# Optimization experiments

Measured on AMD Instinct MI355X. Metric: run time of the kernel, lower is better.

Reference implementation:

```python
import jax, jax.numpy as jnp
import numpy as np

B=1; NW=8; SEG=511; S=NW*(SEG+1); W=256; C=S//W; H=12; D=64; DM=768; FF=3072; V=50265; L=12; OUT=128; G=NW
SCALE = float(1.0/np.sqrt(D))
GPOS = np.arange(NW)*(S//NW)                      # global (CLS) token positions
IDX = np.arange(C)[:,None]*W + np.arange(3*W)[None,:]   # [C,3W] gather into padded key seq
_band = np.abs(np.arange(3*W)[None,:]-np.arange(W)[:,None]-W) <= W   # [W,3W] |rel|<=W band
_kpos = IDX - W
LMASK = _band[None] & ((_kpos>=0)&(_kpos<S))[:,None,:]  # [C,W,3W]

def _ln(x, s, b):
    m = jnp.mean(x, -1, keepdims=True)
    v = jnp.mean((x-m)**2, -1, keepdims=True)
    return (x-m)*jax.lax.rsqrt(v+1e-5)*s + b

def _layer(h, Wq,bq,Wk,bk,Wv,bv,Wo,bo,Wqg,bqg,Wkg,bkg,Wvg,bvg,l1s,l1b,W1,b1,W2,b2,l2s,l2b):
    hd = lambda z: z.reshape(B,S,H,D).transpose(0,2,1,3)   # [B,H,S,D]
    q = hd(h@Wq+bq)*SCALE
    k = hd(h@Wk+bk); v = hd(h@Wv+bv)
    kc = jnp.pad(k, ((0,0),(0,0),(W,W),(0,0)))[:,:,IDX]    # [B,H,C,3W,D]
    vc = jnp.pad(v, ((0,0),(0,0),(W,W),(0,0)))[:,:,IDX]
    qc = q.reshape(B,H,C,W,D)
    # banded local scores + scores to global keys, joint softmax (HF longformer style)
    sl = jnp.where(LMASK, jnp.einsum('bhcqd,bhckd->bhcqk', qc, kc), -1e9)
    sg = jnp.einsum('bhcqd,bhgd->bhcqg', qc, k[:,:,GPOS])
    a = jax.nn.softmax(jnp.concatenate([sg, sl], -1), -1)  # [B,H,C,W,G+3W]
    out = jnp.einsum('bhcqg,bhgd->bhcqd', a[..., :G], v[:,:,GPOS]) \
        + jnp.einsum('bhcqk,bhckd->bhcqd', a[..., G:], vc)
    out = out.reshape(B,H,S,D)
    # global tokens: full attention with separate global projections, overwrite their outputs
    qg = (h[:,GPOS]@Wqg+bqg).reshape(B,G,H,D).transpose(0,2,1,3)*SCALE
    ag = jax.nn.softmax(jnp.einsum('bhgd,bhsd->bhgs', qg, hd(h@Wkg+bkg)), -1)
    out = out.at[:,:,GPOS,:].set(jnp.einsum('bhgs,bhsd->bhgd', ag, hd(h@Wvg+bvg)))
    y = out.transpose(0,2,1,3).reshape(B,S,DM)@Wo + bo
    h = _ln(h + y, l1s, l1b)
    return _ln(h + jax.nn.gelu(h@W1+b1)@W2 + b2, l2s, l2b)

def setup_inputs() -> dict:
    keys = iter(jax.random.split(jax.random.key(0), 64))
    p = lambda *s: jax.random.normal(next(keys), s, jnp.float32)*0.02
    d = {"x": jax.random.randint(next(keys), (B, NW*SEG), 0, V),
         "word_emb": p(V, DM), "pos_emb": p(S, DM),
         "emb_ln_s": jnp.ones((DM,)), "emb_ln_b": jnp.zeros((DM,))}
    for n in ["Wq","Wk","Wv","Wo","Wqg","Wkg","Wvg"]:
        d[n] = p(L, DM, DM); d["b"+n[1:]] = jnp.zeros((L, DM))
    d["ln1_s"]=jnp.ones((L,DM)); d["ln1_b"]=jnp.zeros((L,DM))
    d["W1"]=p(L,DM,FF); d["b1"]=jnp.zeros((L,FF))
    d["W2"]=p(L,FF,DM); d["b2"]=jnp.zeros((L,DM))
    d["ln2_s"]=jnp.ones((L,DM)); d["ln2_b"]=jnp.zeros((L,DM))
    d["Wout"]=p(DM,OUT); d["bout"]=jnp.zeros((OUT,))
    return d

def reference(x, word_emb, pos_emb, emb_ln_s, emb_ln_b, Wq, bq, Wk, bk, Wv, bv, Wo, bo,
              Wqg, bqg, Wkg, bkg, Wvg, bvg, ln1_s, ln1_b, W1, b1, W2, b2, ln2_s, ln2_b,
              Wout, bout):
    # prepend CLS (id 0) per window -> S=4096 token ids
    ids = jnp.concatenate([jnp.zeros((B, NW, 1), x.dtype), x.reshape(B, NW, SEG)], 2).reshape(B, S)
    h = _ln(word_emb[ids] + pos_emb[None], emb_ln_s, emb_ln_b)
    for l in range(L):
        h = _layer(h, Wq[l],bq[l],Wk[l],bk[l],Wv[l],bv[l],Wo[l],bo[l],
                   Wqg[l],bqg[l],Wkg[l],bkg[l],Wvg[l],bvg[l],
                   ln1_s[l],ln1_b[l],W1[l],b1[l],W2[l],b2[l],ln2_s[l],ln2_b[l])
    return h[:, GPOS] @ Wout + bout   # cls_pooling + output head: [B, NW, OUT]
```

## Files before the change

### kernel.cpp

```cpp
#include <hip/hip_runtime.h>
#include <hip/hip_bf16.h>


typedef unsigned short u16;
typedef __attribute__((ext_vector_type(4))) float floatx4;
typedef __attribute__((ext_vector_type(4))) unsigned int uintx4;
typedef __attribute__((ext_vector_type(8))) short bf16x8;
typedef __attribute__((ext_vector_type(4))) u16 u16x4;

#define S_LEN 4096
#define QKVG_N 4608
#define NL 12

__device__ inline u16 f2bf(float x) {
    union { __hip_bfloat16 b; u16 u; } cv;
    cv.b = __float2bfloat16(x);
    return cv.u;
}
__device__ inline float bf2f(u16 u) {
    union { float f; unsigned int i; } c; c.i = ((unsigned int)u) << 16; return c.f;
}
__device__ inline float gelu_f(float x) {
    float x3 = x * x * x;
    return 0.5f * x * (1.0f + tanhf(0.7978845608028654f * (x + 0.044715f * x3)));
}

#define GLDS16(g, l)                                                              \
    __builtin_amdgcn_global_load_lds(                                             \
        (const __attribute__((address_space(1))) unsigned int*)(g),               \
        (__attribute__((address_space(3))) unsigned int*)(l), 16, 0, 0)

__global__ __launch_bounds__(256) void prep_weights_k(
    const float* __restrict__ Wq0, const float* __restrict__ Wk0, const float* __restrict__ Wv0,
    const float* __restrict__ Wkg0, const float* __restrict__ Wvg0, const float* __restrict__ Wqg0,
    const float* __restrict__ Wo0, const float* __restrict__ W10, const float* __restrict__ W20,
    const float* __restrict__ bq0, const float* __restrict__ bk0, const float* __restrict__ bv0,
    const float* __restrict__ bkg0, const float* __restrict__ bvg0, const float* __restrict__ bqg0,
    u16* __restrict__ wTall, float* __restrict__ bcatall)
{
    const int t = threadIdx.x;
    const int bid = blockIdx.x;
    if (bid >= 6480) {
        int i = (bid - 6480) * 256 + t;
        int l = i / 4608, j = i - l * 4608;
        float v;
        if (j < 768)       v = bq0[l * 768 + j];
        else if (j < 1536) v = bk0[l * 768 + j - 768];
        else if (j < 2304) v = bv0[l * 768 + j - 1536];
        else if (j < 3072) v = bkg0[l * 768 + j - 2304];
        else if (j < 3840) v = bvg0[l * 768 + j - 3072];
        else               v = bqg0[l * 768 + j - 3840];
        bcatall[(size_t)l * 4608 + j] = v;
        return;
    }

    const int l = bid / 540, b = bid - l * 540;
    const size_t sqo = (size_t)l * 589824;
    const size_t sff = (size_t)l * 2359296;
    u16* wq = wTall + (size_t)l * 8847360;
    const float* src; u16* dst; int K, N, kt, ns;
    if (b < 216) {
        int m = b / 36, s = b - m * 36;
        src = ((m == 0) ? Wq0 : (m == 1) ? Wk0 : (m == 2) ? Wv0 :
               (m == 3) ? Wkg0 : (m == 4) ? Wvg0 : Wqg0) + sqo;
        dst = wq + (size_t)m * 589824;
        K = 768; N = 768; kt = s / 3; ns = s - kt * 3;
    } else if (b < 252) {
        int s = b - 216; src = Wo0 + sqo; dst = wq + 3538944;
        K = 768; N = 768; kt = s / 3; ns = s - kt * 3;
    } else if (b < 396) {
        int s = b - 252; src = W10 + sff; dst = wq + 4128768;
        K = 768; N = 3072; kt = s / 12; ns = s - kt * 12;
    } else {
        int s = b - 396; src = W20 + sff; dst = wq + 6488064;
        K = 3072; N = 768; kt = s / 3; ns = s - kt * 3;
    }
    const int k0 = kt * 64, n0b = ns * 256;

    __shared__ float tb[2][64][65];
    const int r = t >> 4, c4 = (t & 15) * 4;
    const float* srow = src + (size_t)k0 * N + n0b;
    floatx4 rg[4];
    #pragma unroll
    for (int j = 0; j < 4; j++)
        rg[j] = *(const floatx4*)&srow[(size_t)(r + 16 * j) * N + c4];

    #pragma unroll
    for (int s4 = 0; s4 < 4; ++s4) {
        float (*tbb)[65] = tb[s4 & 1];
        #pragma unroll
        for (int j = 0; j < 4; j++) {
            int kk = r + 16 * j;
            #pragma unroll
            for (int i = 0; i < 4; i++) tbb[c4 + i][kk] = rg[j][i];
        }
        __syncthreads();
        if (s4 < 3) {
            #pragma unroll
            for (int j = 0; j < 4; j++)
                rg[j] = *(const floatx4*)&srow[(size_t)(r + 16 * j) * N + (s4 + 1) * 64 + c4];
        }
        int n0 = n0b + s4 * 64;
        #pragma unroll
        for (int j = 0; j < 4; j++) {
            int n = r + 16 * j;
            u16x4 o;
            #pragma unroll
            for (int i = 0; i < 4; i++) o[i] = f2bf(tbb[n][c4 + i]);
            *(u16x4*)&dst[(size_t)(n0 + n) * K + k0 + c4] = o;
        }
    }
}

template <int ACT, int WF, int WB, int SKIPQG, int WVT, int SPLITB>
__global__ __launch_bounds__(256, 3) void gemm_k(
    const u16* __restrict__ A, const u16* __restrict__ Bt,
    const float* __restrict__ bias,
    float* __restrict__ Cf, u16* __restrict__ Cb, u16* __restrict__ vTg,
    int N, int K, int lda, int ldb)
{
    int lin = blockIdx.y * 32 + blockIdx.x;
    int qq = gridDim.y << 2;
    int wg = (lin & 7) * qq + (lin >> 3);
    int bx = wg & 31, by = wg >> 5;
    if (SKIPQG && by >= 30 && (bx & 3) != 0) return;
    int bm = bx * 128, bn = by * 128;
    const int zoff = SPLITB ? blockIdx.z : 0;
    const u16* Ab = A + (size_t)zoff * K;
    const u16* Bb = Bt + (size_t)zoff * K;
    float* Cfz = WF ? Cf + (size_t)zoff * S_LEN * N : (float*)nullptr;

    __shared__ __align__(16) u16 As[128][64];
    __shared__ __align__(16) u16 Bs[128][64];
    int t = threadIdx.x, lane = t & 63, wv = t >> 6;
    int wm = (wv >> 1) * 64, wn = (wv & 1) * 64;
    int srow = t >> 3, scol = (t & 7) * 8;
    int fr = lane & 15, fo = (lane >> 4) * 8;

    floatx4 acc[4][4];
    #pragma unroll
    for (int i = 0; i < 4; i++)
        #pragma unroll
        for (int j = 0; j < 4; j++) acc[i][j] = (floatx4){0.f, 0.f, 0.f, 0.f};

    const int nk = K >> 6;
    for (int kt = 0; kt < nk; ++kt) {
        const u16* ag = Ab + (size_t)(bm + srow) * lda + kt * 64 + scol;
        const u16* bg = Bb + (size_t)(bn + srow) * ldb + kt * 64 + scol;
        #pragma unroll
        for (int c = 0; c < 4; ++c) {
            GLDS16(ag + (size_t)(32 * c) * lda, &As[srow + 32 * c][scol]);
            GLDS16(bg + (size_t)(32 * c) * ldb, &Bs[srow + 32 * c][scol]);
        }
        __syncthreads();
        #pragma unroll
        for (int ks = 0; ks < 2; ++ks) {
            bf16x8 af[4], bfr[4];
            #pragma unroll
            for (int i = 0; i < 4; i++) af[i]  = *(const bf16x8*)&As[wm + i * 16 + fr][ks * 32 + fo];
            #pragma unroll
            for (int i = 0; i < 4; i++) bfr[i] = *(const bf16x8*)&Bs[wn + i * 16 + fr][ks * 32 + fo];
            #pragma unroll
            for (int i = 0; i < 4; i++)
                #pragma unroll
                for (int j = 0; j < 4; j++)
                    acc[i][j] = __builtin_amdgcn_mfma_f32_16x16x32_bf16(af[i], bfr[j], acc[i][j], 0, 0, 0);
        }
        __syncthreads();
    }

    int dr = (lane >> 4) * 4, dc = lane & 15;
    #pragma unroll
    for (int i = 0; i < 4; i++) {
        #pragma unroll
        for (int j = 0; j < 4; j++) {
            int r0 = bm + wm + i * 16 + dr;
            int cc = bn + wn + j * 16 + dc;
            float bsv = (!SPLITB || blockIdx.z == 0) ? bias[cc] : 0.f;
            u16x4 tv;
            #pragma unroll
            for (int r = 0; r < 4; r++) {
                float v = acc[i][j][r] + bsv;
                if (ACT == 1) v = gelu_f(v);
                if (WF) Cfz[(size_t)(r0 + r) * N + cc] = v;
                if (WB) { u16 b = f2bf(v); Cb[(size_t)(r0 + r) * N + cc] = b; tv[r] = b; }
            }
            if (WVT && cc >= 1536 && cc < 2304)
                *(u16x4*)&vTg[(size_t)(cc - 1536) * 4096 + r0] = tv;
        }
    }
}

__global__ __launch_bounds__(256) void attn_local_k(
    const u16* __restrict__ qkvg, const u16* __restrict__ vTg, u16* __restrict__ aob)
{
    int lin = blockIdx.y * 64 + blockIdx.x;
    int wg = (lin & 7) * 96 + (lin >> 3);
    const int qb = wg & 63, hh = wg >> 6;
    const int t = threadIdx.x, lane = t & 63, w = t >> 6;
    const int g = lane >> 4, qi = lane & 15;
    __shared__ __align__(16) u16 ks[64][72];
    __shared__ __align__(16) u16 vt[64][72];
    __shared__ __align__(16) u16 pbuf[4][16][40];

    const int q0w = qb * 64 + w * 16;
    const int sq = q0w + qi;

    bf16x8 qf0, qf1;
    {
        const u16* qp = qkvg + (size_t)(q0w + qi) * QKVG_N + hh * 64 + g * 8;
        qf0 = *(const bf16x8*)qp;
        qf1 = *(const bf16x8*)(qp + 32);
    }

    floatx4 acc[4];
    #pragma unroll
    for (int i = 0; i < 4; i++) acc[i] = (floatx4){0.f, 0.f, 0.f, 0.f};
    float mrun = -1e30f, lrun = 0.f;

    for (int tile = 0; tile <= 9; ++tile) {
        const int kbase = qb * 64 - 256 + (tile - 1) * 64;
        if (tile > 0 && (kbase < 0 || kbase >= S_LEN)) continue;
        __syncthreads();
        if (tile == 0) {
            for (int i = t; i < 576; i += 256) ((uintx4*)vt)[i] = (uintx4){0, 0, 0, 0};
            __syncthreads();
            if (t < 64) {
                int gg = t >> 3, d0 = (t & 7) * 8;
                *(uintx4*)&ks[gg][d0] =
                    *(const uintx4*)(qkvg + (size_t)(gg * 512) * QKVG_N + 768 + hh * 64 + d0);
            }
            for (int e = t; e < 512; e += 256) {
                int d = e >> 3, gg = e & 7;
                vt[d][gg] = vTg[(size_t)(hh * 64 + d) * 4096 + gg * 512];
            }
        } else {
            for (int c = t; c < 512; c += 256) {
                int r = c >> 3, c0 = (c & 7) * 8;
                *(uintx4*)&ks[r][c0] =
                    *(const uintx4*)(qkvg + (size_t)(kbase + r) * QKVG_N + 768 + hh * 64 + c0);
                *(uintx4*)&vt[r][c0] =
                    *(const uintx4*)(vTg + (size_t)(hh * 64 + r) * 4096 + kbase + c0);
            }
        }
        __syncthreads();

        const bool gt = (tile == 0);
        const bool edge = (tile == 1) | (tile == 9);
        const int ng = gt ? 1 : 2;
        for (int kg2 = 0; kg2 < ng; ++kg2) {
            floatx4 sf[2];
            sf[1] = (floatx4){0.f, 0.f, 0.f, 0.f};
            {
                bf16x8 ka0 = *(const bf16x8*)&ks[kg2 * 32 + qi][g * 8];
                bf16x8 ka1 = *(const bf16x8*)&ks[kg2 * 32 + qi][32 + g * 8];
                floatx4 z = (floatx4){0.f, 0.f, 0.f, 0.f};
                z = __builtin_amdgcn_mfma_f32_16x16x32_bf16(ka0, qf0, z, 0, 0, 0);
                sf[0] = __builtin_amdgcn_mfma_f32_16x16x32_bf16(ka1, qf1, z, 0, 0, 0);
            }
            if (!gt) {
                bf16x8 kb0 = *(const bf16x8*)&ks[kg2 * 32 + 16 + qi][g * 8];
                bf16x8 kb1 = *(const bf16x8*)&ks[kg2 * 32 + 16 + qi][32 + g * 8];
                floatx4 z = (floatx4){0.f, 0.f, 0.f, 0.f};
                z = __builtin_amdgcn_mfma_f32_16x16x32_bf16(kb0, qf0, z, 0, 0, 0);
                sf[1] = __builtin_amdgcn_mfma_f32_16x16x32_bf16(kb1, qf1, z, 0, 0, 0);
            }
            float p8[8];
            float mloc = -1e30f;
            #pragma unroll
            for (int f = 0; f < 2; ++f)
                #pragma unroll
                for (int r = 0; r < 4; ++r) {
                    int kl = kg2 * 32 + f * 16 + g * 4 + r;
                    float sc = sf[f][r] * 0.125f;
                    if (gt) {
                        if (kl >= 8) sc = -1e30f;
                    } else if (edge) {
                        int dd = kbase + kl - sq;
                        if (dd > 256 || dd < -256) sc = -1e30f;
                    }
                    p8[f * 4 + r] = sc;
                    mloc = fmaxf(mloc, sc);
                }
            mloc = fmaxf(mloc, __shfl_xor(mloc, 16));
            mloc = fmaxf(mloc, __shfl_xor(mloc, 32));
            float mnew = fmaxf(mrun, mloc);
            float alpha = __expf(mrun - mnew);
            mrun = mnew;
            float ls = 0.f;
            #pragma unroll
            for (int i = 0; i < 8; ++i) { float p = __expf(p8[i] - mnew); p8[i] = p; ls += p; }
            ls += __shfl_xor(ls, 16);
            ls += __shfl_xor(ls, 32);
            lrun = lrun * alpha + ls;
            u16x4 w0, w1;
            #pragma unroll
            for (int r = 0; r < 4; ++r) { w0[r] = f2bf(p8[r]); w1[r] = f2bf(p8[4 + r]); }
            *(u16x4*)&pbuf[w][qi][g * 4] = w0;
            *(u16x4*)&pbuf[w][qi][16 + g * 4] = w1;
            float al[4];
            #pragma unroll
            for (int r = 0; r < 4; ++r) al[r] = __shfl(alpha, g * 4 + r);
            #pragma unroll
            for (int dt = 0; dt < 4; ++dt)
                #pragma unroll
                for (int r = 0; r < 4; ++r) acc[dt][r] *= al[r];
            bf16x8 pf = *(const bf16x8*)&pbuf[w][qi][g * 8];
            #pragma unroll
            for (int dt = 0; dt < 4; ++dt) {
                bf16x8 vb = *(const bf16x8*)&vt[dt * 16 + qi][kg2 * 32 + g * 8];
                acc[dt] = __builtin_amdgcn_mfma_f32_16x16x32_bf16(pf, vb, acc[dt], 0, 0, 0);
            }
        }
    }

    float inv = 1.f / lrun;
    float li[4];
    #pragma unroll
    for (int r = 0; r < 4; ++r) li[r] = __shfl(inv, g * 4 + r);
    #pragma unroll
    for (int dt = 0; dt < 4; ++dt)
        #pragma unroll
        for (int r = 0; r < 4; ++r) {
            int s = q0w + g * 4 + r;
            aob[(size_t)s * 768 + hh * 64 + dt * 16 + qi] = f2bf(acc[dt][r] * li[r]);
        }
}

#define BLOCK_MEANVAR(sum, sq, mean, inv)                                        \
    {                                                                            \
        for (int o_ = 32; o_ > 0; o_ >>= 1) {                                    \
            sum += __shfl_down(sum, o_); sq += __shfl_down(sq, o_);              \
        }                                                                        \
        __shared__ float rs_[4], rq_[4];                                         \
        if ((threadIdx.x & 63) == 0) { rs_[threadIdx.x >> 6] = sum; rq_[threadIdx.x >> 6] = sq; } \
        __syncthreads();                                                         \
        float S_ = rs_[0] + rs_[1] + rs_[2] + rs_[3];                            \
        float Q_ = rq_[0] + rq_[1] + rq_[2] + rq_[3];                            \
        mean = S_ * (1.f / 768.f);                                               \
        float var_ = Q_ * (1.f / 768.f) - mean * mean;                           \
        inv = rsqrtf(var_ + 1e-5f);                                              \
    }

__global__ __launch_bounds__(256) void embed_ln_k(
    const int* __restrict__ x, const float* __restrict__ wemb, const float* __restrict__ pemb,
    const float* __restrict__ gs, const float* __restrict__ gb,
    float* __restrict__ hf, u16* __restrict__ hb)
{
    int s = blockIdx.x, t = threadIdx.x;
    int w = s >> 9, p = s & 511;
    int id = (p == 0) ? 0 : x[w * 511 + p - 1];
    float v[3], sum = 0.f, sq = 0.f;
    #pragma unroll
    for (int r = 0; r < 3; r++) {
        int d = t + r * 256;
        float e = wemb[(size_t)id * 768 + d] + pemb[(size_t)s * 768 + d];
        v[r] = e; sum += e; sq += e * e;
    }
    float mean, inv;
    BLOCK_MEANVAR(sum, sq, mean, inv)
    #pragma unroll
    for (int r = 0; r < 3; r++) {
        int d = t + r * 256;
        float y = (v[r] - mean) * inv * gs[d] + gb[d];
        hf[(size_t)s * 768 + d] = y;
        hb[(size_t)s * 768 + d] = f2bf(y);
    }
}

__global__ __launch_bounds__(192) void ln_resid_k(
    const float* __restrict__ xa, const float* __restrict__ yf,
    const float* __restrict__ gs, const float* __restrict__ gb,
    float* __restrict__ of, u16* __restrict__ ob)
{
    int s = blockIdx.x, t = threadIdx.x;
    size_t off = (size_t)s * 768 + t * 4;
    floatx4 v = *(const floatx4*)(xa + off);
    #pragma unroll
    for (int z = 0; z < 4; z++) {
        floatx4 b = *(const floatx4*)(yf + (size_t)z * 4096 * 768 + off);
        #pragma unroll
        for (int i = 0; i < 4; i++) v[i] += b[i];
    }
    float sum = v[0] + v[1] + v[2] + v[3];
    float sq = v[0] * v[0] + v[1] * v[1] + v[2] * v[2] + v[3] * v[3];
    #pragma unroll
    for (int o = 32; o > 0; o >>= 1) {
        sum += __shfl_down(sum, o); sq += __shfl_down(sq, o);
    }
    __shared__ float rs_[3], rq_[3];
    if ((t & 63) == 0) { rs_[t >> 6] = sum; rq_[t >> 6] = sq; }
    __syncthreads();
    float S = rs_[0] + rs_[1] + rs_[2];
    float Q = rq_[0] + rq_[1] + rq_[2];
    float mean = S * (1.f / 768.f);
    float inv = rsqrtf(Q * (1.f / 768.f) - mean * mean + 1e-5f);
    floatx4 g4 = *(const floatx4*)(gs + t * 4);
    floatx4 b4 = *(const floatx4*)(gb + t * 4);
    floatx4 y;
    u16x4 o4;
    #pragma unroll
    for (int i = 0; i < 4; i++) {
        y[i] = (v[i] - mean) * inv * g4[i] + b4[i];
        o4[i] = f2bf(y[i]);
    }
    *(floatx4*)(of + off) = y;
    *(u16x4*)(ob + off) = o4;
}

__global__ __launch_bounds__(256) void attn_gpart_k(
    const u16* __restrict__ qkvg,
    float* __restrict__ pacc, float* __restrict__ pm, float* __restrict__ pl)
{
    const int hh = blockIdx.x, ck = blockIdx.y;
    const int t = threadIdx.x;
    __shared__ float qs[8][64];
    __shared__ __align__(16) u16 ks[128][72];
    __shared__ __align__(16) u16 vs[128][64];
    __shared__ float sc[8][128];
    __shared__ float mred[8], lred[8];

    for (int i = t; i < 512; i += 256) {
        int g = i >> 6, d = i & 63;
        qs[g][d] = bf2f(qkvg[(size_t)(g * 512) * QKVG_N + 3840 + hh * 64 + d]) * 0.125f;
    }
    const int s0 = ck * 128;
    for (int u = t; u < 1024; u += 256) {
        int r = u >> 3, c = u & 7;
        const u16* src = qkvg + (size_t)(s0 + r) * QKVG_N + hh * 64 + c * 8;
        *(uintx4*)&ks[r][c * 8] = *(const uintx4*)(src + 2304);
        *(uintx4*)&vs[r][c * 8] = *(const uintx4*)(src + 3072);
    }
    __syncthreads();

    {
        int key = t & 127, q0 = (t >> 7) * 4;
        float a[4] = {0.f, 0.f, 0.f, 0.f};
        #pragma unroll
        for (int c = 0; c < 8; ++c) {
            uintx4 pk = *(const uintx4*)&ks[key][c * 8];
            const u16* uu = (const u16*)&pk;
            #pragma unroll
            for (int e = 0; e < 8; ++e) {
                float kv = bf2f(uu[e]);
                #pragma unroll
                for (int q = 0; q < 4; ++q) a[q] += kv * qs[q0 + q][c * 8 + e];
            }
        }
        #pragma unroll
        for (int q = 0; q < 4; ++q) sc[q0 + q][key] = a[q];
    }
    __syncthreads();

    {
        int q = t >> 5, lq = t & 31;
        float m = -1e30f;
        #pragma unroll
        for (int i = 0; i < 4; ++i) m = fmaxf(m, sc[q][lq + i * 32]);
        #pragma unroll
        for (int o = 1; o < 32; o <<= 1) m = fmaxf(m, __shfl_xor(m, o));
        float ls = 0.f;
        #pragma unroll
        for (int i = 0; i < 4; ++i) {
            float p = __expf(sc[q][lq + i * 32] - m);
            sc[q][lq + i * 32] = p; ls += p;
        }
        #pragma unroll
        for (int o = 1; o < 32; o <<= 1) ls += __shfl_xor(ls, o);
        if (lq == 0) { mred[q] = m; lred[q] = ls; }
    }
    __syncthreads();

    {
        int d = t & 63, qb = t >> 6;
        float a0 = 0.f, a1 = 0.f;
        #pragma unroll 4
        for (int s = 0; s < 128; ++s) {
            float v = bf2f(vs[s][d]);
            a0 += sc[qb][s] * v;
            a1 += sc[qb + 4][s] * v;
        }
        float* pb = pacc + (((size_t)hh * 32 + ck) * 8) * 64;
        pb[qb * 64 + d] = a0;
        pb[(qb + 4) * 64 + d] = a1;
        if (t < 8) {
            pm[((size_t)hh * 32 + ck) * 8 + t] = mred[t];
            pl[((size_t)hh * 32 + ck) * 8 + t] = lred[t];
        }
    }
}

__global__ __launch_bounds__(64) void attn_gred_k(
    const float* __restrict__ pacc, const float* __restrict__ pm,
    const float* __restrict__ pl, u16* __restrict__ aob)
{
    int hh = blockIdx.x, gq = blockIdx.y;
    int d = threadIdx.x;
    float M = -1e30f;
    #pragma unroll 4
    for (int c = 0; c < 32; ++c)
        M = fmaxf(M, pm[((size_t)hh * 32 + c) * 8 + gq]);
    float L = 0.f, o = 0.f;
    #pragma unroll 4
    for (int c = 0; c < 32; ++c) {
        float w = __expf(pm[((size_t)hh * 32 + c) * 8 + gq] - M);
        L += pl[((size_t)hh * 32 + c) * 8 + gq] * w;
        o += w * pacc[(((size_t)hh * 32 + c) * 8 + gq) * 64 + d];
    }
    aob[(size_t)(gq * 512) * 768 + hh * 64 + d] = f2bf(o / L);
}

__global__ __launch_bounds__(128) void head_k(
    const float* __restrict__ hf, const float* __restrict__ Wout,
    const float* __restrict__ bout, float* __restrict__ out)
{
    int g = blockIdx.x, n = threadIdx.x;
    __shared__ float hsh[768];
    for (int i = n; i < 768; i += 128) hsh[i] = hf[(size_t)(g * 512) * 768 + i];
    __syncthreads();
    float a = 0.f;
    #pragma unroll 4
    for (int k = 0; k < 768; k++) a += hsh[k] * Wout[k * 128 + n];
    out[g * 128 + n] = a + bout[n];
}

extern "C" void kernel_launch(void* const* d_in, const int* in_sizes, int n_in,
                              void* d_out, int out_size, void* d_ws, size_t ws_size,
                              hipStream_t stream)
{
    (void)in_sizes; (void)n_in; (void)out_size; (void)ws_size;
    const int*   x    = (const int*)  d_in[0];
    const float* wemb = (const float*)d_in[1];
    const float* pemb = (const float*)d_in[2];
    const float* elns = (const float*)d_in[3];
    const float* elnb = (const float*)d_in[4];
    const float* Wq   = (const float*)d_in[5];
    const float* bq   = (const float*)d_in[6];
    const float* Wk   = (const float*)d_in[7];
    const float* bk   = (const float*)d_in[8];
    const float* Wv   = (const float*)d_in[9];
    const float* bv   = (const float*)d_in[10];
    const float* Wo   = (const float*)d_in[11];
    const float* bo   = (const float*)d_in[12];
    const float* Wqg  = (const float*)d_in[13];
    const float* bqg  = (const float*)d_in[14];
    const float* Wkg  = (const float*)d_in[15];
    const float* bkg  = (const float*)d_in[16];
    const float* Wvg  = (const float*)d_in[17];
    const float* bvg  = (const float*)d_in[18];
    const float* l1s  = (const float*)d_in[19];
    const float* l1b  = (const float*)d_in[20];
    const float* W1   = (const float*)d_in[21];
    const float* b1   = (const float*)d_in[22];
    const float* W2   = (const float*)d_in[23];
    const float* b2   = (const float*)d_in[24];
    const float* l2s  = (const float*)d_in[25];
    const float* l2b  = (const float*)d_in[26];
    const float* Wout = (const float*)d_in[27];
    const float* boutp= (const float*)d_in[28];

    char* W = (char*)d_ws;
    float* hf    = (float*)(W);
    u16*   hb    = (u16*)  (W + 12582912);
    u16*   qkvg  = (u16*)  (W + 18874368);
    u16*   ff1b  = (u16*)  (W + 18874368);
    u16*   vTg   = (u16*)  (W + 56623104);
    u16*   aob   = (u16*)  (W + 62914560);
    float* yf    = (float*)(W + 69206016);
    float* pacc  = (float*)(W + 119537664);
    float* pmw   = (float*)(W + 120324096);
    float* plw   = (float*)(W + 120336384);
    float* bcatall = (float*)(W + 120348672);
    u16*   wTall = (u16*)  (W + 120569856);

    prep_weights_k<<<6696, 256, 0, stream>>>(
        Wq, Wk, Wv, Wkg, Wvg, Wqg, Wo, W1, W2,
        bq, bk, bv, bkg, bvg, bqg, wTall, bcatall);

    embed_ln_k<<<4096, 256, 0, stream>>>(x, wemb, pemb, elns, elnb, hf, hb);

    for (int l = 0; l < NL; ++l) {
        u16* wTl      = wTall + (size_t)l * 8847360;
        u16* wqkvgT_l = wTl;
        u16* woT_l    = wTl + 3538944;
        u16* w1T_l    = woT_l + 589824;
        u16* w2T_l    = w1T_l + 2359296;
        float* bcat_l = bcatall + (size_t)l * 4608;
        const float* bo_l  = bo  + (size_t)l * 768;
        const float* b1_l  = b1  + (size_t)l * 3072;
        const float* b2_l  = b2  + (size_t)l * 768;
        const float* l1s_l = l1s + (size_t)l * 768;
        const float* l1b_l = l1b + (size_t)l * 768;
        const float* l2s_l = l2s + (size_t)l * 768;
        const float* l2b_l = l2b + (size_t)l * 768;

        gemm_k<0, 0, 1, 1, 1, 0><<<dim3(32, 36), 256, 0, stream>>>(
            hb, wqkvgT_l, bcat_l, (float*)nullptr, qkvg, vTg, QKVG_N, 768, 768, 768);

        attn_local_k<<<dim3(64, 12), 256, 0, stream>>>(qkvg, vTg, aob);

        attn_gpart_k<<<dim3(12, 32), 256, 0, stream>>>(qkvg, pacc, pmw, plw);
        attn_gred_k<<<dim3(12, 8), 64, 0, stream>>>(pacc, pmw, plw, aob);

        gemm_k<0, 1, 0, 0, 0, 1><<<dim3(32, 6, 4), 256, 0, stream>>>(
            aob, woT_l, bo_l, yf, (u16*)nullptr, (u16*)nullptr, 768, 192, 768, 768);
        ln_resid_k<<<4096, 192, 0, stream>>>(hf, yf, l1s_l, l1b_l, hf, hb);

        gemm_k<1, 0, 1, 0, 0, 0><<<dim3(32, 24), 256, 0, stream>>>(
            hb, w1T_l, b1_l, (float*)nullptr, ff1b, (u16*)nullptr, 3072, 768, 768, 768);
        gemm_k<0, 1, 0, 0, 0, 1><<<dim3(32, 6, 4), 256, 0, stream>>>(
            ff1b, w2T_l, b2_l, yf, (u16*)nullptr, (u16*)nullptr, 768, 768, 3072, 3072);
        ln_resid_k<<<4096, 192, 0, stream>>>(hf, yf, l2s_l, l2b_l, hf, hb);
    }

    head_k<<<8, 128, 0, stream>>>(hf, Wout, boutp, (float*)d_out);
}
```

Before: 2.838 ms.

## Reduce split-K GEMM partials with atomics into one zeroed buffer

Split-K GEMM blocks now atomically add their partial results into a single fp32 output buffer instead of writing separate per-split slices. The residual layernorm reads that one buffer and zeroes it afterwards for reuse, and the embedding kernel zeroes it on first use. This cuts the partial-sum write and read traffic, since four separate slices are no longer summed. In exchange it adds atomic contention and makes the summation order, and so the result, nondeterministic.

```diff
diff --git a/kernel.cpp b/kernel.cpp
--- a/kernel.cpp
+++ b/kernel.cpp
@@ -128,7 +128,6 @@
     const int zoff = SPLITB ? blockIdx.z : 0;
     const u16* Ab = A + (size_t)zoff * K;
     const u16* Bb = Bt + (size_t)zoff * K;
-    float* Cfz = WF ? Cf + (size_t)zoff * S_LEN * N : (float*)nullptr;
 
     __shared__ __align__(16) u16 As[128][64];
     __shared__ __align__(16) u16 Bs[128][64];
@@ -182,7 +181,10 @@
             for (int r = 0; r < 4; r++) {
                 float v = acc[i][j][r] + bsv;
                 if (ACT == 1) v = gelu_f(v);
-                if (WF) Cfz[(size_t)(r0 + r) * N + cc] = v;
+                if (WF) {
+                    if (SPLITB) atomicAdd(&Cf[(size_t)(r0 + r) * N + cc], v);
+                    else        Cf[(size_t)(r0 + r) * N + cc] = v;
+                }
                 if (WB) { u16 b = f2bf(v); Cb[(size_t)(r0 + r) * N + cc] = b; tv[r] = b; }
             }
             if (WVT && cc >= 1536 && cc < 2304)
@@ -327,61 +329,20 @@
         }
 }
 
-#define BLOCK_MEANVAR(sum, sq, mean, inv)                                        \
-    {                                                                            \
-        for (int o_ = 32; o_ > 0; o_ >>= 1) {                                    \
-            sum += __shfl_down(sum, o_); sq += __shfl_down(sq, o_);              \
-        }                                                                        \
-        __shared__ float rs_[4], rq_[4];                                         \
-        if ((threadIdx.x & 63) == 0) { rs_[threadIdx.x >> 6] = sum; rq_[threadIdx.x >> 6] = sq; } \
-        __syncthreads();                                                         \
-        float S_ = rs_[0] + rs_[1] + rs_[2] + rs_[3];                            \
-        float Q_ = rq_[0] + rq_[1] + rq_[2] + rq_[3];                            \
-        mean = S_ * (1.f / 768.f);                                               \
-        float var_ = Q_ * (1.f / 768.f) - mean * mean;                           \
-        inv = rsqrtf(var_ + 1e-5f);                                              \
-    }
-
-__global__ __launch_bounds__(256) void embed_ln_k(
+__global__ __launch_bounds__(192) void embed_ln_k(
     const int* __restrict__ x, const float* __restrict__ wemb, const float* __restrict__ pemb,
     const float* __restrict__ gs, const float* __restrict__ gb,
-    float* __restrict__ hf, u16* __restrict__ hb)
+    float* __restrict__ hf, u16* __restrict__ hb, float* __restrict__ yz)
 {
     int s = blockIdx.x, t = threadIdx.x;
     int w = s >> 9, p = s & 511;
     int id = (p == 0) ? 0 : x[w * 511 + p - 1];
-    float v[3], sum = 0.f, sq = 0.f;
-    #pragma unroll
-    for (int r = 0; r < 3; r++) {
-        int d = t + r * 256;
-        float e = wemb[(size_t)id * 768 + d] + pemb[(size_t)s * 768 + d];
-        v[r] = e; sum += e; sq += e * e;
-    }
-    float mean, inv;
-    BLOCK_MEANVAR(sum, sq, mean, inv)
-    #pragma unroll
-    for (int r = 0; r < 3; r++) {
-        int d = t + r * 256;
-        float y = (v[r] - mean) * inv * gs[d] + gb[d];
-        hf[(size_t)s * 768 + d] = y;
-        hb[(size_t)s * 768 + d] = f2bf(y);
-    }
-}
-
-__global__ __launch_bounds__(192) void ln_resid_k(
-    const float* __restrict__ xa, const float* __restrict__ yf,
-    const float* __restrict__ gs, const float* __restrict__ gb,
-    float* __restrict__ of, u16* __restrict__ ob)
-{
-    int s = blockIdx.x, t = threadIdx.x;
     size_t off = (size_t)s * 768 + t * 4;
-    floatx4 v = *(const floatx4*)(xa + off);
-    #pragma unroll
-    for (int z = 0; z < 4; z++) {
-        floatx4 b = *(const floatx4*)(yf + (size_t)z * 4096 * 768 + off);
-        #pragma unroll
-        for (int i = 0; i < 4; i++) v[i] += b[i];
-    }
+    floatx4 a = *(const floatx4*)(wemb + (size_t)id * 768 + t * 4);
+    floatx4 b = *(const floatx4*)(pemb + off);
+    floatx4 v;
+    #pragma unroll
+    for (int i = 0; i < 4; i++) v[i] = a[i] + b[i];
     float sum = v[0] + v[1] + v[2] + v[3];
     float sq = v[0] * v[0] + v[1] * v[1] + v[2] * v[2] + v[3] * v[3];
     #pragma unroll
@@ -404,7 +365,47 @@
         y[i] = (v[i] - mean) * inv * g4[i] + b4[i];
         o4[i] = f2bf(y[i]);
     }
-    *(floatx4*)(of + off) = y;
+    *(floatx4*)(hf + off) = y;
+    *(u16x4*)(hb + off) = o4;
+    *(floatx4*)(yz + off) = (floatx4){0.f, 0.f, 0.f, 0.f};
+}
+
+__global__ __launch_bounds__(192) void ln_resid_k(
+    const float* __restrict__ xa, float* __restrict__ y,
+    const float* __restrict__ gs, const float* __restrict__ gb,
+    float* __restrict__ of, u16* __restrict__ ob)
+{
+    int s = blockIdx.x, t = threadIdx.x;
+    size_t off = (size_t)s * 768 + t * 4;
+    floatx4 a = *(const floatx4*)(xa + off);
+    floatx4 b = *(const floatx4*)(y + off);
+    floatx4 v;
+    #pragma unroll
+    for (int i = 0; i < 4; i++) v[i] = a[i] + b[i];
+    *(floatx4*)(y + off) = (floatx4){0.f, 0.f, 0.f, 0.f};
+    float sum = v[0] + v[1] + v[2] + v[3];
+    float sq = v[0] * v[0] + v[1] * v[1] + v[2] * v[2] + v[3] * v[3];
+    #pragma unroll
+    for (int o = 32; o > 0; o >>= 1) {
+        sum += __shfl_down(sum, o); sq += __shfl_down(sq, o);
+    }
+    __shared__ float rs_[3], rq_[3];
+    if ((t & 63) == 0) { rs_[t >> 6] = sum; rq_[t >> 6] = sq; }
+    __syncthreads();
+    float S = rs_[0] + rs_[1] + rs_[2];
+    float Q = rq_[0] + rq_[1] + rq_[2];
+    float mean = S * (1.f / 768.f);
+    float inv = rsqrtf(Q * (1.f / 768.f) - mean * mean + 1e-5f);
+    floatx4 g4 = *(const floatx4*)(gs + t * 4);
+    floatx4 b4 = *(const floatx4*)(gb + t * 4);
+    floatx4 yv;
+    u16x4 o4;
+    #pragma unroll
+    for (int i = 0; i < 4; i++) {
+        yv[i] = (v[i] - mean) * inv * g4[i] + b4[i];
+        o4[i] = f2bf(yv[i]);
+    }
+    *(floatx4*)(of + off) = yv;
     *(u16x4*)(ob + off) = o4;
 }
 
@@ -577,7 +578,7 @@
         Wq, Wk, Wv, Wkg, Wvg, Wqg, Wo, W1, W2,
         bq, bk, bv, bkg, bvg, bqg, wTall, bcatall);
 
-    embed_ln_k<<<4096, 256, 0, stream>>>(x, wemb, pemb, elns, elnb, hf, hb);
+    embed_ln_k<<<4096, 192, 0, stream>>>(x, wemb, pemb, elns, elnb, hf, hb, yf);
 
     for (int l = 0; l < NL; ++l) {
         u16* wTl      = wTall + (size_t)l * 8847360;
```

Measured after the change: 3.411 ms. 1.2x slower.
